# Optimization experiments

Hardware: AMD Instinct MI355X
Metric: run time of the kernel (lower is better)

The kernel has to match this reference:

```python
import jax, jax.numpy as jnp
import numpy as np

B, C, S, D = 64, 729, 243, 512


def _layer_norm(x, gamma, beta, eps=1e-5):
    mu = jnp.mean(x, axis=-1, keepdims=True)
    var = jnp.mean((x - mu) ** 2, axis=-1, keepdims=True)
    return (x - mu) * jax.lax.rsqrt(var + eps) * gamma + beta


def setup_inputs() -> dict:
    key = jax.random.key(0)
    ks = jax.random.split(key, 8)
    s = 1.0 / np.sqrt(D)
    return {
        "cand_feat": jax.random.normal(ks[0], (B, C, D), dtype=jnp.float32),
        "set_feat": jax.random.normal(ks[1], (B, S, D), dtype=jnp.float32),
        "W_vc": jax.random.uniform(ks[2], (D, D), jnp.float32, -s, s),
        "b_vc": jnp.zeros((D,), jnp.float32),
        "W_vs": jax.random.uniform(ks[3], (D, D), jnp.float32, -s, s),
        "b_vs": jnp.zeros((D,), jnp.float32),
        "ff_W1": jax.random.uniform(ks[4], (2 * D, D), jnp.float32, -s, s),
        "ff_b1": jnp.zeros((2 * D,), jnp.float32),
        "ff_W2": jax.random.uniform(ks[5], (D, 2 * D), jnp.float32, -1.0 / np.sqrt(2 * D), 1.0 / np.sqrt(2 * D)),
        "ff_b2": jnp.zeros((D,), jnp.float32),
        "g_set": jnp.ones((D,), jnp.float32),
        "be_set": jnp.zeros((D,), jnp.float32),
        "g_cand": jnp.ones((D,), jnp.float32),
        "be_cand": jnp.zeros((D,), jnp.float32),
        "g_ff": jnp.ones((D,), jnp.float32),
        "be_ff": jnp.zeros((D,), jnp.float32),
        "cand_to_set_idx": jax.random.randint(ks[6], (C, 3), 0, S, dtype=jnp.int64 if jax.config.jax_enable_x64 else jnp.int32),
    }


def reference(cand_feat, set_feat, W_vc, b_vc, W_vs, b_vs, ff_W1, ff_b1, ff_W2, ff_b2,
              g_set, be_set, g_cand, be_cand, g_ff, be_ff, cand_to_set_idx):
    b, c, d = cand_feat.shape
    idx = cand_to_set_idx.reshape(-1)  # (2187,)

    cand_msgs = cand_feat @ W_vc.T + b_vc              # (B, 729, D)
    msgs3 = jnp.repeat(cand_msgs, 3, axis=1)           # (B, 2187, D)
    set_updates = jnp.zeros_like(set_feat).at[:, idx, :].add(msgs3) / 9.0
    set_out = _layer_norm(set_feat + set_updates, g_set, be_set)

    # set -> cand: gather 3 sets per candidate, mean, linear
    gathered = set_out[:, idx, :].reshape(b, c, 3, d)  # (B, 729, 3, D)
    cand_updates = gathered.mean(axis=2) @ W_vs.T + b_vs
    cand_h = _layer_norm(cand_feat + cand_updates, g_cand, be_cand)

    # FF block with residual
    ff = jax.nn.relu(cand_h @ ff_W1.T + ff_b1) @ ff_W2.T + ff_b2
    cand_out = _layer_norm(cand_h + ff, g_ff, be_ff)
    return (cand_out, set_out)
```

## Files before the change

### kernel.cpp

```cpp
#include <hip/hip_runtime.h>

using u16 = unsigned short;
using u32 = unsigned int;

typedef __attribute__((ext_vector_type(8))) short bf16x8;
typedef __attribute__((ext_vector_type(4))) float f32x4;
typedef __attribute__((ext_vector_type(8))) u16 u16x8;
typedef __attribute__((ext_vector_type(4))) u16 u16x4;

constexpr int NB = 64, NC = 729, NS = 243, ND = 512, ND2 = 1024;
constexpr int MS = NB * NS;
constexpr int MC = NB * NC;
constexpr int MCH = MC / 3;

__device__ __forceinline__ u16 f2bf(float f) {
  u32 u = __builtin_bit_cast(u32, f);
  return (u16)((u + 0x7fffu + ((u >> 16) & 1u)) >> 16);
}
__device__ __forceinline__ float bf2f(u16 h) {
  return __builtin_bit_cast(float, (u32)h << 16);
}
__device__ __forceinline__ void gload16(const void* g, void* l) {
  __builtin_amdgcn_global_load_lds((const __attribute__((address_space(1))) u32*)g,
                                   (__attribute__((address_space(3))) u32*)l, 16, 0, 0);
}

__global__ __launch_bounds__(256) void cast_bf16_k(const float* __restrict__ in,
                                                   u16* __restrict__ out, int n4) {
  int i = blockIdx.x * 256 + threadIdx.x;
  if (i >= n4) return;
  f32x4 v = ((const f32x4*)in)[i];
  u16x4 o;
  o.x = f2bf(v.x); o.y = f2bf(v.y); o.z = f2bf(v.z); o.w = f2bf(v.w);
  ((u16x4*)out)[i] = o;
}

__global__ __launch_bounds__(1024) void build_csr_k(const int* __restrict__ idx,
                                                    int* __restrict__ offs,
                                                    int* __restrict__ list) {
  constexpr int NE = 3 * NC;
  constexpr int NCH = (NE + 63) / 64;
  __shared__ int sidx[NE];
  __shared__ int lrank[NE];
  __shared__ int hist[NCH][NS];
  __shared__ int scan[256];
  __shared__ int soffs[NS];
  const int t = threadIdx.x;
  const int wv = t >> 6, ln = t & 63;

  for (int e = t; e < NE; e += 1024) sidx[e] = idx[e];
  for (int i = t; i < NCH * NS; i += 1024) (&hist[0][0])[i] = 0;
  __syncthreads();

  for (int c = wv; c < NCH; c += 16) {
    int e = c * 64 + ln;
    int s = (e < NE) ? sidx[e] : -1;
    int rank = 0, tot = 0;
#pragma unroll
    for (int l2 = 0; l2 < 64; ++l2) {
      int v = __shfl(s, l2);
      bool m = (v == s) && (s >= 0);
      rank += (m && (l2 < ln)) ? 1 : 0;
      tot  += m ? 1 : 0;
    }
    if (e < NE) {
      lrank[e] = rank;
      if (rank == 0) hist[c][s] = tot;
    }
  }
  __syncthreads();

  int mycnt = 0;
  if (t < NS) {
    int run = 0;
#pragma unroll 5
    for (int c = 0; c < NCH; ++c) { int v = hist[c][t]; hist[c][t] = run; run += v; }
    mycnt = run;
  }
  if (t < 256) scan[t] = (t < NS) ? mycnt : 0;
  __syncthreads();

  for (int d = 1; d < 256; d <<= 1) {
    int v = 0;
    if (t < 256 && t >= d) v = scan[t - d];
    __syncthreads();
    if (t < 256) scan[t] += v;
    __syncthreads();
  }
  if (t < NS) {
    soffs[t] = scan[t] - mycnt;
    offs[t] = scan[t] - mycnt;
  }
  if (t == 0) offs[NS] = NE;
  __syncthreads();

  for (int e = t; e < NE; e += 1024) {
    int s = sidx[e];
    list[soffs[s] + hist[e >> 6][s] + lrank[e]] = e / 3;
  }
}

__global__ __launch_bounds__(256) void agg_k(const float* __restrict__ cand_feat,
                                             const int* __restrict__ offs,
                                             const int* __restrict__ list,
                                             u16* __restrict__ agg) {
  int row = blockIdx.x * 4 + (threadIdx.x >> 6);
  if (row >= MS) return;
  int lane = threadIdx.x & 63;
  int b = row / NS, s = row - b * NS;
  int e0 = offs[s], e1 = offs[s + 1];
  const float* base = cand_feat + (size_t)b * NC * ND + lane * 8;
  f32x4 a0 = {0.f, 0.f, 0.f, 0.f}, a1 = {0.f, 0.f, 0.f, 0.f};
  for (int e = e0; e < e1; ++e) {
    const float* p = base + (size_t)list[e] * ND;
    a0 += *(const f32x4*)p;
    a1 += *(const f32x4*)(p + 4);
  }
  u16x8 o;
  o[0] = f2bf(a0.x); o[1] = f2bf(a0.y); o[2] = f2bf(a0.z); o[3] = f2bf(a0.w);
  o[4] = f2bf(a1.x); o[5] = f2bf(a1.y); o[6] = f2bf(a1.z); o[7] = f2bf(a1.w);
  *(u16x8*)(agg + (size_t)row * ND + lane * 8) = o;
}

template <int EP>
__global__ __launch_bounds__(256, 3) void gemm_k64(const u16* __restrict__ A,
                                                   const u16* __restrict__ Bw,
                                                   void* __restrict__ Out,
                                                   const float* __restrict__ bias,
                                                   int M, int N, int K) {
  constexpr int BK = 64;
  __shared__ u16 lA[128 * BK];
  __shared__ u16 lB[128 * BK];
  const int t = threadIdx.x, wid = t >> 6, lane = t & 63;
  const int NT = N >> 7;
  const int nwg = gridDim.x, cpx = nwg >> 3;
  int wg = blockIdx.x;
  wg = (wg & 7) * cpx + (wg >> 3);
  const int mt = wg / NT, nt = wg % NT;
  const int m0 = mt << 7, n0 = nt << 7;

  const u16* gA[4]; const u16* gB[4]; int ldo[4];
#pragma unroll
  for (int i = 0; i < 4; ++i) {
    int s = i * 256 + t;
    int r = s >> 3, j = s & 7;
    int cj = (j ^ (r & 7)) * 8;
    int ar = m0 + r; if (ar > M - 1) ar = M - 1;
    gA[i] = A + (size_t)ar * K + cj;
    gB[i] = Bw + (size_t)(n0 + r) * K + cj;
    ldo[i] = s * 8;
  }

  const int li = lane & 15, g0 = lane >> 4;
  const int wr = wid >> 1, wc = wid & 1;
  int aOff[4], bOff[4];
#pragma unroll
  for (int i = 0; i < 4; ++i) {
    int rowA = wr * 64 + i * 16 + li;
    int rowB = wc * 64 + i * 16 + li;
    aOff[i] = rowA * 64 + ((g0 ^ (li & 7)) << 3);
    bOff[i] = rowB * 64 + ((g0 ^ (li & 7)) << 3);
  }

  f32x4 acc[4][4] = {};

  for (int kt = 0; kt < K; kt += BK) {
#pragma unroll
    for (int i = 0; i < 4; ++i) gload16(gA[i], lA + ldo[i]);
#pragma unroll
    for (int i = 0; i < 4; ++i) gload16(gB[i], lB + ldo[i]);
#pragma unroll
    for (int i = 0; i < 4; ++i) { gA[i] += BK; gB[i] += BK; }
    __syncthreads();
#pragma unroll
    for (int kk = 0; kk < 2; ++kk) {
      bf16x8 af[4], bfr[4];
#pragma unroll
      for (int i = 0; i < 4; ++i) {
        af[i]  = *(const bf16x8*)(lA + (aOff[i] ^ (kk << 5)));
        bfr[i] = *(const bf16x8*)(lB + (bOff[i] ^ (kk << 5)));
      }
#pragma unroll
      for (int mi = 0; mi < 4; ++mi)
#pragma unroll
        for (int ni = 0; ni < 4; ++ni)
          acc[mi][ni] = __builtin_amdgcn_mfma_f32_16x16x32_bf16(af[mi], bfr[ni], acc[mi][ni], 0, 0, 0);
    }
    __syncthreads();
  }

  const int rb = m0 + wr * 64 + (g0 << 2);
  const int cb = n0 + wc * 64 + li;
  if (EP == 0) {
    float* O = (float*)Out;
#pragma unroll
    for (int mi = 0; mi < 4; ++mi)
#pragma unroll
      for (int ni = 0; ni < 4; ++ni) {
        int cc = cb + ni * 16;
#pragma unroll
        for (int r = 0; r < 4; ++r) {
          int rr = rb + mi * 16 + r;
          if (rr < M) O[(size_t)rr * N + cc] = acc[mi][ni][r];
        }
      }
  } else {
    u16* O = (u16*)Out;
    float bv[4];
#pragma unroll
    for (int ni = 0; ni < 4; ++ni) bv[ni] = bias[cb + ni * 16];
#pragma unroll
    for (int mi = 0; mi < 4; ++mi)
#pragma unroll
      for (int ni = 0; ni < 4; ++ni) {
        int cc = cb + ni * 16;
#pragma unroll
        for (int r = 0; r < 4; ++r) {
          int rr = rb + mi * 16 + r;
          float v = acc[mi][ni][r] + bv[ni];
          if (EP == 1) v = fmaxf(v, 0.0f);
          if (rr < M) O[(size_t)rr * N + cc] = f2bf(v);
        }
      }
  }
}

__global__ __launch_bounds__(256) void set_ln_k(const float* __restrict__ u1,
                                                const float* __restrict__ set_feat,
                                                const int* __restrict__ offs,
                                                const float* __restrict__ b_vc,
                                                const float* __restrict__ gam,
                                                const float* __restrict__ bet,
                                                float* __restrict__ set_out,
                                                u16* __restrict__ set_out_bf) {
  int row = blockIdx.x * 4 + (threadIdx.x >> 6);
  if (row >= MS) return;
  int lane = threadIdx.x & 63;
  int s = row % NS;
  float c9 = (float)(offs[s + 1] - offs[s]) * (1.0f / 9.0f);
  size_t base = (size_t)row * ND + lane * 8;
  f32x4 u0 = *(const f32x4*)(u1 + base),       u1b = *(const f32x4*)(u1 + base + 4);
  f32x4 s0 = *(const f32x4*)(set_feat + base), s1  = *(const f32x4*)(set_feat + base + 4);
  f32x4 b0 = *(const f32x4*)(b_vc + lane * 8), b1  = *(const f32x4*)(b_vc + lane * 8 + 4);
  f32x4 x0 = s0 + u0 * (1.0f / 9.0f) + b0 * c9;
  f32x4 x1 = s1 + u1b * (1.0f / 9.0f) + b1 * c9;
  float sm = 0.f, sq = 0.f;
#pragma unroll
  for (int i = 0; i < 4; ++i) { sm += x0[i] + x1[i]; sq += x0[i] * x0[i] + x1[i] * x1[i]; }
#pragma unroll
  for (int m = 32; m; m >>= 1) { sm += __shfl_xor(sm, m); sq += __shfl_xor(sq, m); }
  float mu = sm * (1.0f / ND);
  float rs = rsqrtf(sq * (1.0f / ND) - mu * mu + 1e-5f);
  f32x4 g0 = *(const f32x4*)(gam + lane * 8), g1 = *(const f32x4*)(gam + lane * 8 + 4);
  f32x4 e0 = *(const f32x4*)(bet + lane * 8), e1 = *(const f32x4*)(bet + lane * 8 + 4);
  f32x4 y0, y1; u16x8 ob;
#pragma unroll
  for (int i = 0; i < 4; ++i) {
    y0[i] = (x0[i] - mu) * rs * g0[i] + e0[i];
    y1[i] = (x1[i] - mu) * rs * g1[i] + e1[i];
    ob[i] = f2bf(y0[i]); ob[i + 4] = f2bf(y1[i]);
  }
  *(f32x4*)(set_out + base) = y0;
  *(f32x4*)(set_out + base + 4) = y1;
  *(u16x8*)(set_out_bf + base) = ob;
}

__global__ __launch_bounds__(256) void cand_ln_k(const float* __restrict__ cand_feat,
                                                 const float* __restrict__ proj,
                                                 const int* __restrict__ cidx,
                                                 const float* __restrict__ b_vs,
                                                 const float* __restrict__ gam,
                                                 const float* __restrict__ bet,
                                                 u16* __restrict__ cand_h) {
  int row = blockIdx.x * 4 + (threadIdx.x >> 6);
  if (row >= MC) return;
  int lane = threadIdx.x & 63;
  int b = row / NC, c = row - b * NC;
  int i0 = cidx[c * 3], i1 = cidx[c * 3 + 1], i2 = cidx[c * 3 + 2];
  const float* pb = proj + (size_t)b * NS * ND + lane * 8;
  f32x4 p00 = *(const f32x4*)(pb + (size_t)i0 * ND), p01 = *(const f32x4*)(pb + (size_t)i0 * ND + 4);
  f32x4 p10 = *(const f32x4*)(pb + (size_t)i1 * ND), p11 = *(const f32x4*)(pb + (size_t)i1 * ND + 4);
  f32x4 p20 = *(const f32x4*)(pb + (size_t)i2 * ND), p21 = *(const f32x4*)(pb + (size_t)i2 * ND + 4);
  size_t base = (size_t)row * ND + lane * 8;
  f32x4 c0 = *(const f32x4*)(cand_feat + base), c1 = *(const f32x4*)(cand_feat + base + 4);
  f32x4 v0 = *(const f32x4*)(b_vs + lane * 8),  v1 = *(const f32x4*)(b_vs + lane * 8 + 4);
  const float third = 1.0f / 3.0f;
  f32x4 x0 = c0 + (p00 + p10 + p20) * third + v0;
  f32x4 x1 = c1 + (p01 + p11 + p21) * third + v1;
  float sm = 0.f, sq = 0.f;
#pragma unroll
  for (int i = 0; i < 4; ++i) { sm += x0[i] + x1[i]; sq += x0[i] * x0[i] + x1[i] * x1[i]; }
#pragma unroll
  for (int m = 32; m; m >>= 1) { sm += __shfl_xor(sm, m); sq += __shfl_xor(sq, m); }
  float mu = sm * (1.0f / ND);
  float rs = rsqrtf(sq * (1.0f / ND) - mu * mu + 1e-5f);
  f32x4 g0 = *(const f32x4*)(gam + lane * 8), g1 = *(const f32x4*)(gam + lane * 8 + 4);
  f32x4 e0 = *(const f32x4*)(bet + lane * 8), e1 = *(const f32x4*)(bet + lane * 8 + 4);
  u16x8 ob;
#pragma unroll
  for (int i = 0; i < 4; ++i) {
    ob[i]     = f2bf((x0[i] - mu) * rs * g0[i] + e0[i]);
    ob[i + 4] = f2bf((x1[i] - mu) * rs * g1[i] + e1[i]);
  }
  *(u16x8*)(cand_h + base) = ob;
}

__global__ __launch_bounds__(256) void ln_ff_k(const u16* __restrict__ h2b,
                                               const u16* __restrict__ resid,
                                               const float* __restrict__ gam,
                                               const float* __restrict__ bet,
                                               float* __restrict__ out, int nrows) {
  int row = blockIdx.x * 4 + (threadIdx.x >> 6);
  if (row >= nrows) return;
  int lane = threadIdx.x & 63;
  size_t base = (size_t)row * ND + lane * 8;
  u16x8 ha = *(const u16x8*)(h2b + base);
  u16x8 ra = *(const u16x8*)(resid + base);
  float x[8];
  float sm = 0.f, sq = 0.f;
#pragma unroll
  for (int i = 0; i < 8; ++i) {
    x[i] = bf2f(ha[i]) + bf2f(ra[i]);
    sm += x[i]; sq += x[i] * x[i];
  }
#pragma unroll
  for (int m = 32; m; m >>= 1) { sm += __shfl_xor(sm, m); sq += __shfl_xor(sq, m); }
  float mu = sm * (1.0f / ND);
  float rs = rsqrtf(sq * (1.0f / ND) - mu * mu + 1e-5f);
  f32x4 g0 = *(const f32x4*)(gam + lane * 8), g1 = *(const f32x4*)(gam + lane * 8 + 4);
  f32x4 e0 = *(const f32x4*)(bet + lane * 8), e1 = *(const f32x4*)(bet + lane * 8 + 4);
  f32x4 y0, y1;
#pragma unroll
  for (int i = 0; i < 4; ++i) {
    y0[i] = (x[i] - mu) * rs * g0[i] + e0[i];
    y1[i] = (x[i + 4] - mu) * rs * g1[i] + e1[i];
  }
  *(f32x4*)(out + base) = y0;
  *(f32x4*)(out + base + 4) = y1;
}

extern "C" void kernel_launch(void* const* d_in, const int* in_sizes, int n_in,
                              void* d_out, int out_size, void* d_ws, size_t ws_size,
                              hipStream_t stream) {
  const float* cand_feat = (const float*)d_in[0];
  const float* set_feat  = (const float*)d_in[1];
  const float* W_vc  = (const float*)d_in[2];
  const float* b_vc  = (const float*)d_in[3];
  const float* W_vs  = (const float*)d_in[4];
  const float* b_vs  = (const float*)d_in[5];
  const float* ff_W1 = (const float*)d_in[6];
  const float* ff_b1 = (const float*)d_in[7];
  const float* ff_W2 = (const float*)d_in[8];
  const float* ff_b2 = (const float*)d_in[9];
  const float* g_set  = (const float*)d_in[10];
  const float* be_set = (const float*)d_in[11];
  const float* g_cand = (const float*)d_in[12];
  const float* be_cand= (const float*)d_in[13];
  const float* g_ff   = (const float*)d_in[14];
  const float* be_ff  = (const float*)d_in[15];
  const int*   cidx   = (const int*)d_in[16];
  (void)in_sizes; (void)n_in; (void)out_size; (void)ws_size;

  char* ws = (char*)d_ws;
  u16* w_vc_b = (u16*)(ws + 0);
  u16* w_vs_b = (u16*)(ws + (512 << 10));
  u16* w1_b   = (u16*)(ws + (1 << 20));
  u16* w2_b   = (u16*)(ws + (2 << 20));
  int* offs   = (int*)(ws + (3 << 20));
  int* list   = (int*)(ws + (3 << 20) + 4096);
  u16* setb   = (u16*)(ws + (4 << 20));
  u16* candh  = (u16*)(ws + (20 << 20));
  u16* h2chunk = setb;

  float* out_cand = (float*)d_out;
  float* out_set  = out_cand + (size_t)MC * ND;
  u16*   agg  = (u16*)out_set;
  float* u1   = out_cand;
  float* proj = out_cand;
  u16*   h1   = (u16*)out_cand;

  cast_bf16_k<<<(ND * ND / 4 + 255) / 256, 256, 0, stream>>>(W_vc, w_vc_b, ND * ND / 4);
  cast_bf16_k<<<(ND * ND / 4 + 255) / 256, 256, 0, stream>>>(W_vs, w_vs_b, ND * ND / 4);
  cast_bf16_k<<<(ND2 * ND / 4 + 255) / 256, 256, 0, stream>>>(ff_W1, w1_b, ND2 * ND / 4);
  cast_bf16_k<<<(ND * ND2 / 4 + 255) / 256, 256, 0, stream>>>(ff_W2, w2_b, ND * ND2 / 4);
  build_csr_k<<<1, 1024, 0, stream>>>(cidx, offs, list);
  agg_k<<<(MS + 3) / 4, 256, 0, stream>>>(cand_feat, offs, list, agg);
  gemm_k64<0><<<122 * 4, 256, 0, stream>>>(agg, w_vc_b, u1, nullptr, MS, ND, ND);
  set_ln_k<<<(MS + 3) / 4, 256, 0, stream>>>(u1, set_feat, offs, b_vc, g_set, be_set, out_set, setb);
  gemm_k64<0><<<122 * 4, 256, 0, stream>>>(setb, w_vs_b, proj, nullptr, MS, ND, ND);
  cand_ln_k<<<(MC + 3) / 4, 256, 0, stream>>>(cand_feat, proj, cidx, b_vs, g_cand, be_cand, candh);
  gemm_k64<1><<<365 * 8, 256, 0, stream>>>(candh, w1_b, h1, ff_b1, MC, ND2, ND);
  for (int c = 0; c < 3; ++c) {
    const u16* h1c   = h1 + (size_t)c * MCH * ND2;
    const u16* residc= candh + (size_t)c * MCH * ND;
    float* outc      = out_cand + (size_t)c * MCH * ND;
    gemm_k64<2><<<122 * 4, 256, 0, stream>>>(h1c, w2_b, h2chunk, ff_b2, MCH, ND, ND2);
    ln_ff_k<<<(MCH + 3) / 4, 256, 0, stream>>>(h2chunk, residc, g_ff, be_ff, outc, MCH);
  }
}
```

Measured before the change: 373.0 us.

## Store intermediate GEMM outputs in bf16, merge weight casts, unchunk FF2 GEMM

The four weight cast launches become one kernel. The two D×D GEMM outputs (u1, proj) are written as bf16 instead of fp32, which halves their write and read traffic in the LayerNorm kernels. The three-chunk FF2 GEMM plus LN loop is replaced by a single full-size GEMM into a separate workspace buffer and one LN launch. The GEMM's occupancy hint goes from 3 to 4 blocks, and the XCD block remap now handles grids that are not multiples of 8. The risks are lower precision in the intermediates, higher register pressure, and a larger workspace that must fit.

```diff
diff --git a/kernel.cpp b/kernel.cpp
--- a/kernel.cpp
+++ b/kernel.cpp
@@ -11,7 +11,6 @@
 constexpr int NB = 64, NC = 729, NS = 243, ND = 512, ND2 = 1024;
 constexpr int MS = NB * NS;
 constexpr int MC = NB * NC;
-constexpr int MCH = MC / 3;
 
 __device__ __forceinline__ u16 f2bf(float f) {
   u32 u = __builtin_bit_cast(u32, f);
@@ -25,14 +24,22 @@
                                    (__attribute__((address_space(3))) u32*)l, 16, 0, 0);
 }
 
-__global__ __launch_bounds__(256) void cast_bf16_k(const float* __restrict__ in,
-                                                   u16* __restrict__ out, int n4) {
+__global__ __launch_bounds__(256) void cast_all_k(const float* __restrict__ s0,
+                                                  const float* __restrict__ s1,
+                                                  const float* __restrict__ s2,
+                                                  const float* __restrict__ s3,
+                                                  u16* __restrict__ d0, u16* __restrict__ d1,
+                                                  u16* __restrict__ d2, u16* __restrict__ d3) {
   int i = blockIdx.x * 256 + threadIdx.x;
-  if (i >= n4) return;
-  f32x4 v = ((const f32x4*)in)[i];
+  const float* s; u16* d; int off;
+  if (i < 65536)       { s = s0; d = d0; off = i; }
+  else if (i < 131072) { s = s1; d = d1; off = i - 65536; }
+  else if (i < 262144) { s = s2; d = d2; off = i - 131072; }
+  else                 { s = s3; d = d3; off = i - 262144; }
+  f32x4 v = ((const f32x4*)s)[off];
   u16x4 o;
   o.x = f2bf(v.x); o.y = f2bf(v.y); o.z = f2bf(v.z); o.w = f2bf(v.w);
-  ((u16x4*)out)[i] = o;
+  ((u16x4*)d)[off] = o;
 }
 
 __global__ __launch_bounds__(1024) void build_csr_k(const int* __restrict__ idx,
@@ -123,7 +130,7 @@
 }
 
 template <int EP>
-__global__ __launch_bounds__(256, 3) void gemm_k64(const u16* __restrict__ A,
+__global__ __launch_bounds__(256, 4) void gemm_k64(const u16* __restrict__ A,
                                                    const u16* __restrict__ Bw,
                                                    void* __restrict__ Out,
                                                    const float* __restrict__ bias,
@@ -133,9 +140,10 @@
   __shared__ u16 lB[128 * BK];
   const int t = threadIdx.x, wid = t >> 6, lane = t & 63;
   const int NT = N >> 7;
-  const int nwg = gridDim.x, cpx = nwg >> 3;
-  int wg = blockIdx.x;
-  wg = (wg & 7) * cpx + (wg >> 3);
+  const int nwg = gridDim.x;
+  int wg;
+  { int q = nwg >> 3, r = nwg & 7, x = blockIdx.x & 7, p = blockIdx.x >> 3;
+    wg = (x < r ? x * (q + 1) : r * (q + 1) + (x - r) * q) + p; }
   const int mt = wg / NT, nt = wg % NT;
   const int m0 = mt << 7, n0 = nt << 7;
 
@@ -208,7 +216,7 @@
     u16* O = (u16*)Out;
     float bv[4];
 #pragma unroll
-    for (int ni = 0; ni < 4; ++ni) bv[ni] = bias[cb + ni * 16];
+    for (int ni = 0; ni < 4; ++ni) bv[ni] = (EP == 3) ? 0.0f : bias[cb + ni * 16];
 #pragma unroll
     for (int mi = 0; mi < 4; ++mi)
 #pragma unroll
@@ -225,7 +233,7 @@
   }
 }
 
-__global__ __launch_bounds__(256) void set_ln_k(const float* __restrict__ u1,
+__global__ __launch_bounds__(256) void set_ln_k(const u16* __restrict__ u1,
                                                 const float* __restrict__ set_feat,
                                                 const int* __restrict__ offs,
                                                 const float* __restrict__ b_vc,
@@ -239,11 +247,15 @@
   int s = row % NS;
   float c9 = (float)(offs[s + 1] - offs[s]) * (1.0f / 9.0f);
   size_t base = (size_t)row * ND + lane * 8;
-  f32x4 u0 = *(const f32x4*)(u1 + base),       u1b = *(const f32x4*)(u1 + base + 4);
+  u16x8 ua = *(const u16x8*)(u1 + base);
   f32x4 s0 = *(const f32x4*)(set_feat + base), s1  = *(const f32x4*)(set_feat + base + 4);
   f32x4 b0 = *(const f32x4*)(b_vc + lane * 8), b1  = *(const f32x4*)(b_vc + lane * 8 + 4);
-  f32x4 x0 = s0 + u0 * (1.0f / 9.0f) + b0 * c9;
-  f32x4 x1 = s1 + u1b * (1.0f / 9.0f) + b1 * c9;
+  f32x4 x0, x1;
+#pragma unroll
+  for (int i = 0; i < 4; ++i) {
+    x0[i] = s0[i] + bf2f(ua[i]) * (1.0f / 9.0f) + b0[i] * c9;
+    x1[i] = s1[i] + bf2f(ua[i + 4]) * (1.0f / 9.0f) + b1[i] * c9;
+  }
   float sm = 0.f, sq = 0.f;
 #pragma unroll
   for (int i = 0; i < 4; ++i) { sm += x0[i] + x1[i]; sq += x0[i] * x0[i] + x1[i] * x1[i]; }
@@ -266,7 +278,7 @@
 }
 
 __global__ __launch_bounds__(256) void cand_ln_k(const float* __restrict__ cand_feat,
-                                                 const float* __restrict__ proj,
+                                                 const u16* __restrict__ proj,
                                                  const int* __restrict__ cidx,
                                                  const float* __restrict__ b_vs,
                                                  const float* __restrict__ gam,
@@ -277,16 +289,20 @@
   int lane = threadIdx.x & 63;
   int b = row / NC, c = row - b * NC;
   int i0 = cidx[c * 3], i1 = cidx[c * 3 + 1], i2 = cidx[c * 3 + 2];
-  const float* pb = proj + (size_t)b * NS * ND + lane * 8;
-  f32x4 p00 = *(const f32x4*)(pb + (size_t)i0 * ND), p01 = *(const f32x4*)(pb + (size_t)i0 * ND + 4);
-  f32x4 p10 = *(const f32x4*)(pb + (size_t)i1 * ND), p11 = *(const f32x4*)(pb + (size_t)i1 * ND + 4);
-  f32x4 p20 = *(const f32x4*)(pb + (size_t)i2 * ND), p21 = *(const f32x4*)(pb + (size_t)i2 * ND + 4);
+  const u16* pb = proj + (size_t)b * NS * ND + lane * 8;
+  u16x8 p0 = *(const u16x8*)(pb + (size_t)i0 * ND);
+  u16x8 p1 = *(const u16x8*)(pb + (size_t)i1 * ND);
+  u16x8 p2 = *(const u16x8*)(pb + (size_t)i2 * ND);
   size_t base = (size_t)row * ND + lane * 8;
   f32x4 c0 = *(const f32x4*)(cand_feat + base), c1 = *(const f32x4*)(cand_feat + base + 4);
   f32x4 v0 = *(const f32x4*)(b_vs + lane * 8),  v1 = *(const f32x4*)(b_vs + lane * 8 + 4);
   const float third = 1.0f / 3.0f;
-  f32x4 x0 = c0 + (p00 + p10 + p20) * third + v0;
-  f32x4 x1 = c1 + (p01 + p11 + p21) * third + v1;
+  f32x4 x0, x1;
+#pragma unroll
+  for (int i = 0; i < 4; ++i) {
+    x0[i] = c0[i] + (bf2f(p0[i]) + bf2f(p1[i]) + bf2f(p2[i])) * third + v0[i];
+    x1[i] = c1[i] + (bf2f(p0[i + 4]) + bf2f(p1[i + 4]) + bf2f(p2[i + 4])) * third + v1[i];
+  }
   float sm = 0.f, sq = 0.f;
 #pragma unroll
   for (int i = 0; i < 4; ++i) { sm += x0[i] + x1[i]; sq += x0[i] * x0[i] + x1[i] * x1[i]; }
@@ -370,31 +386,23 @@
   int* list   = (int*)(ws + (3 << 20) + 4096);
   u16* setb   = (u16*)(ws + (4 << 20));
   u16* candh  = (u16*)(ws + (20 << 20));
-  u16* h2chunk = setb;
+  u16* h2b    = (u16*)(ws + (size_t)(68 << 20));
 
   float* out_cand = (float*)d_out;
   float* out_set  = out_cand + (size_t)MC * ND;
   u16*   agg  = (u16*)out_set;
-  float* u1   = out_cand;
-  float* proj = out_cand;
+  u16*   u1   = (u16*)out_cand;
+  u16*   proj = (u16*)out_cand;
   u16*   h1   = (u16*)out_cand;
 
-  cast_bf16_k<<<(ND * ND / 4 + 255) / 256, 256, 0, stream>>>(W_vc, w_vc_b, ND * ND / 4);
-  cast_bf16_k<<<(ND * ND / 4 + 255) / 256, 256, 0, stream>>>(W_vs, w_vs_b, ND * ND / 4);
-  cast_bf16_k<<<(ND2 * ND / 4 + 255) / 256, 256, 0, stream>>>(ff_W1, w1_b, ND2 * ND / 4);
-  cast_bf16_k<<<(ND * ND2 / 4 + 255) / 256, 256, 0, stream>>>(ff_W2, w2_b, ND * ND2 / 4);
+  cast_all_k<<<1536, 256, 0, stream>>>(W_vc, W_vs, ff_W1, ff_W2, w_vc_b, w_vs_b, w1_b, w2_b);
   build_csr_k<<<1, 1024, 0, stream>>>(cidx, offs, list);
   agg_k<<<(MS + 3) / 4, 256, 0, stream>>>(cand_feat, offs, list, agg);
-  gemm_k64<0><<<122 * 4, 256, 0, stream>>>(agg, w_vc_b, u1, nullptr, MS, ND, ND);
+  gemm_k64<3><<<122 * 4, 256, 0, stream>>>(agg, w_vc_b, u1, nullptr, MS, ND, ND);
   set_ln_k<<<(MS + 3) / 4, 256, 0, stream>>>(u1, set_feat, offs, b_vc, g_set, be_set, out_set, setb);
-  gemm_k64<0><<<122 * 4, 256, 0, stream>>>(setb, w_vs_b, proj, nullptr, MS, ND, ND);
+  gemm_k64<3><<<122 * 4, 256, 0, stream>>>(setb, w_vs_b, proj, nullptr, MS, ND, ND);
   cand_ln_k<<<(MC + 3) / 4, 256, 0, stream>>>(cand_feat, proj, cidx, b_vs, g_cand, be_cand, candh);
   gemm_k64<1><<<365 * 8, 256, 0, stream>>>(candh, w1_b, h1, ff_b1, MC, ND2, ND);
-  for (int c = 0; c < 3; ++c) {
-    const u16* h1c   = h1 + (size_t)c * MCH * ND2;
-    const u16* residc= candh + (size_t)c * MCH * ND;
-    float* outc      = out_cand + (size_t)c * MCH * ND;
-    gemm_k64<2><<<122 * 4, 256, 0, stream>>>(h1c, w2_b, h2chunk, ff_b2, MCH, ND, ND2);
-    ln_ff_k<<<(MCH + 3) / 4, 256, 0, stream>>>(h2chunk, residc, g_ff, be_ff, outc, MCH);
-  }
-}
+  gemm_k64<2><<<365 * 4, 256, 0, stream>>>(h1, w2_b, h2b, ff_b2, MC, ND, ND2);
+  ln_ff_k<<<(MC + 3) / 4, 256, 0, stream>>>(h2b, candh, g_ff, be_ff, out_cand, MC);
+}
```

Measured after the change: 312.8 us. 16.1% less time.
